# Kernel optimization log

Measured on AMD Instinct MI355X. Metric: run time of the kernel, lower is better.

Reference implementation:

```python
import jax, jax.numpy as jnp
import numpy as np

N = 50000
E = 600000
F_IN = 128      # float features (in_channels - 1)
CE = 8          # cell embedding dim
D_IN = F_IN + CE  # 136
C = 128         # out_channels
NUM_CELLS = 854
NEG_SLOPE = 0.2
LN_EPS = 1e-5


def _gat_layer(x, src, dst, W, a_src, a_dst, b):
    """PyG GATConv, heads=1, concat=False, add_self_loops already in src/dst.
    x: [N, Din]; src/dst: [Etot]; W: [Din, C]; a_src/a_dst: [C]; b: [C].
    """
    h = x @ W                               # [N, C]
    alpha_src = h @ a_src                   # [N]
    alpha_dst = h @ a_dst                   # [N]
    e = jax.nn.leaky_relu(alpha_src[src] + alpha_dst[dst], NEG_SLOPE)  # [Etot]
    # segment softmax over edges sharing a destination node
    m = jax.ops.segment_max(e, dst, num_segments=N)    # [N] (every node has a self-loop)
    ex = jnp.exp(e - m[dst])                           # [Etot]
    denom = jax.ops.segment_sum(ex, dst, num_segments=N)  # [N]
    alpha = ex / denom[dst]                            # [Etot]
    out = jax.ops.segment_sum(h[src] * alpha[:, None], dst, num_segments=N)  # [N, C]
    return out + b


def _layer_norm(x, g, b):
    mu = jnp.mean(x, axis=-1, keepdims=True)
    var = jnp.var(x, axis=-1, keepdims=True)
    return (x - mu) * jax.lax.rsqrt(var + LN_EPS) * g + b


def setup_inputs() -> dict:
    key = jax.random.key(0)
    ks = jax.random.split(key, 12)
    x_base = jax.random.normal(ks[0], (N, F_IN), dtype=jnp.float32)
    cell_ids = jax.random.randint(ks[1], (N,), 0, NUM_CELLS, dtype=jnp.int64)
    edge_index = jax.random.randint(ks[2], (2, E), 0, N, dtype=jnp.int64)
    s = 0.05
    cell_emb = jax.random.normal(ks[3], (NUM_CELLS, CE), dtype=jnp.float32)
    W1 = jax.random.normal(ks[4], (D_IN, C), dtype=jnp.float32) * s
    a_src1 = jax.random.normal(ks[5], (C,), dtype=jnp.float32) * s
    a_dst1 = jax.random.normal(ks[6], (C,), dtype=jnp.float32) * s
    b1 = jnp.zeros((C,), dtype=jnp.float32)
    ln_g = jnp.ones((C,), dtype=jnp.float32)
    ln_b = jnp.zeros((C,), dtype=jnp.float32)
    W2 = jax.random.normal(ks[7], (C, C), dtype=jnp.float32) * s
    a_src2 = jax.random.normal(ks[8], (C,), dtype=jnp.float32) * s
    a_dst2 = jax.random.normal(ks[9], (C,), dtype=jnp.float32) * s
    b2 = jnp.zeros((C,), dtype=jnp.float32)
    return {
        "x_base": x_base, "cell_ids": cell_ids, "edge_index": edge_index,
        "cell_emb": cell_emb,
        "W1": W1, "a_src1": a_src1, "a_dst1": a_dst1, "b1": b1,
        "ln_g": ln_g, "ln_b": ln_b,
        "W2": W2, "a_src2": a_src2, "a_dst2": a_dst2, "b2": b2,
    }


def reference(x_base, cell_ids, edge_index, cell_emb,
              W1, a_src1, a_dst1, b1, ln_g, ln_b,
              W2, a_src2, a_dst2, b2):
    # embed cell ids and concat (equiv. to x[:, :-1] + Embedding(x[:, -1]))
    x = jnp.concatenate([x_base, cell_emb[cell_ids]], axis=1)   # [N, 136]
    # PyG GATConv adds self-loops internally
    loops = jnp.arange(N, dtype=edge_index.dtype)
    src = jnp.concatenate([edge_index[0], loops])
    dst = jnp.concatenate([edge_index[1], loops])
    # layer 1 + LN + ELU (dropout inactive in eval mode)
    x = _gat_layer(x, src, dst, W1, a_src1, a_dst1, b1)
    x = jax.nn.elu(_layer_norm(x, ln_g, ln_b))
    # layer 2 (no norm/activation on last layer)
    x = _gat_layer(x, src, dst, W2, a_src2, a_dst2, b2)
    return x
```

## Files before the change

kernel.cpp:

```cpp
#include <hip/hip_runtime.h>
#include <hip/hip_fp16.h>
#include <cstdint>
#include <cstddef>

#define NEG_SLOPE 0.2f
#define LN_EPS 1e-5f

constexpr int BS = 256;
constexpr int EPT = 8;
constexpr int SUBCAP = 96;
constexpr int STRIDE = 96;

typedef _Float16 f16x8 __attribute__((ext_vector_type(8)));
typedef float f32x4 __attribute__((ext_vector_type(4)));

__global__ __launch_bounds__(256) void k_init(
    const int* __restrict__ esrc, const int* __restrict__ edst,
    unsigned int* __restrict__ gb, int* __restrict__ bcnt,
    const float* __restrict__ W1, const float* __restrict__ W2,
    _Float16* __restrict__ Wt1, _Float16* __restrict__ Wt2,
    int e, int nb, int nblk)
{
    int b = blockIdx.x;
    if (b < nblk) {
        __shared__ int lcnt[64];
        int tid = threadIdx.x;
        if (tid < 64) lcnt[tid] = 0;
        __syncthreads();
        int base = b * (BS * EPT) + tid;
        int sv[EPT], dl[EPT], bk[EPT], lp[EPT];
        #pragma unroll
        for (int u = 0; u < EPT; ++u) {
            int i = base + u * BS;
            bool ok = i < e;
            int ii = ok ? i : 0;
            sv[u] = esrc[ii];
            int d = edst[ii];
            dl[u] = d & 1023;
            bk[u] = ok ? (d >> 10) : -1;
        }
        #pragma unroll
        for (int u = 0; u < EPT; ++u)
            lp[u] = (bk[u] >= 0) ? atomicAdd(&lcnt[bk[u]], 1) : SUBCAP;
        __syncthreads();
        if (tid < nb) bcnt[b * nb + tid] = lcnt[tid] < SUBCAP ? lcnt[tid] : SUBCAP;
        #pragma unroll
        for (int u = 0; u < EPT; ++u)
            if (bk[u] >= 0 && lp[u] < SUBCAP)
                gb[((size_t)bk[u] * nblk + b) * SUBCAP + lp[u]] =
                    ((unsigned)dl[u] << 16) | (unsigned)sv[u];
    } else {
        int idx = (b - nblk) * BS + threadIdx.x;
        if (idx < 128 * 160) {
            int nn = idx / 160, k = idx - nn * 160;
            Wt1[idx] = (_Float16)((k < 136) ? W1[(size_t)k * 128 + nn] : 0.f);
        } else if (idx < 128 * 160 + 128 * 128) {
            int j = idx - 128 * 160;
            int nn = j >> 7, k = j & 127;
            Wt2[j] = (_Float16)W2[(size_t)k * 128 + nn];
        }
    }
}

__global__ __launch_bounds__(256) void k_csr_gemm1(
    const unsigned int* __restrict__ gb, const int* __restrict__ bcnt,
    int* __restrict__ cnt, unsigned short* __restrict__ sn,
    const float* __restrict__ x, const int* __restrict__ cid,
    const float* __restrict__ emb,
    const _Float16* __restrict__ Wt1,
    const float* __restrict__ a_src, const float* __restrict__ a_dst,
    _Float16* __restrict__ hb, float* __restrict__ as_, float* __restrict__ ad_,
    int n, int nb, int nblk)
{
    __shared__ float red[2][16][2][2];
    __shared__ int cl[1024];
    int b = blockIdx.x;

    if (b < nb) {
        int tid = threadIdx.x;
        #pragma unroll 4
        for (int i = tid; i < 1024; i += BS) cl[i] = 1;
        __syncthreads();
        for (int blk = tid; blk < nblk; blk += BS) {
            int c = bcnt[blk * nb + b];
            size_t gbase = ((size_t)b * nblk + blk) * SUBCAP;
            for (int j = 0; j < c; j += 8) {
                uint4 p0 = *(const uint4*)(gb + gbase + j);
                uint4 p1 = *(const uint4*)(gb + gbase + j + 4);
                unsigned pk[8] = {p0.x, p0.y, p0.z, p0.w, p1.x, p1.y, p1.z, p1.w};
                int slot[8];
                #pragma unroll
                for (int k = 0; k < 8; ++k)
                    slot[k] = (j + k < c) ? atomicAdd(&cl[pk[k] >> 16], 1) : STRIDE;
                #pragma unroll
                for (int k = 0; k < 8; ++k)
                    if (slot[k] < STRIDE)
                        sn[((size_t)(b * 1024 + (int)(pk[k] >> 16))) * STRIDE + slot[k]] =
                            (unsigned short)(pk[k] & 0xFFFFu);
            }
        }
        __syncthreads();
        for (int i = tid; i < 1024; i += BS) {
            int node = b * 1024 + i;
            if (node < n) {
                int c = cl[i];
                cnt[node] = c < STRIDE ? c : STRIDE;
                sn[(size_t)node * STRIDE] = (unsigned short)node;
            }
        }
        return;
    }

    int idx = b - nb;
    int tid = threadIdx.x;
    int wave = tid >> 6, lane = tid & 63;
    int rg = wave >> 1, ch = wave & 1;
    int r15 = lane & 15, q = lane >> 4;
    int rowBase = idx * 32 + rg * 16;
    int colBase = ch * 64;
    int row = rowBase + r15;
    bool ok = row < n;
    int rl = ok ? row : n - 1;

    f32x4 acc[4] = {};
    const _Float16* Wp[4];
    #pragma unroll
    for (int s = 0; s < 4; ++s)
        Wp[s] = Wt1 + (size_t)(colBase + s * 16 + r15) * 160 + q * 8;
    const float* Xp = x + (size_t)rl * 128 + q * 8;

    #pragma unroll
    for (int k0 = 0; k0 < 128; k0 += 32) {
        f16x8 wv[4];
        #pragma unroll
        for (int s = 0; s < 4; ++s) wv[s] = *(const f16x8*)(Wp[s] + k0);
        float4 xlo = *(const float4*)(Xp + k0);
        float4 xhi = *(const float4*)(Xp + k0 + 4);
        f16x8 xv;
        xv[0] = (_Float16)xlo.x; xv[1] = (_Float16)xlo.y;
        xv[2] = (_Float16)xlo.z; xv[3] = (_Float16)xlo.w;
        xv[4] = (_Float16)xhi.x; xv[5] = (_Float16)xhi.y;
        xv[6] = (_Float16)xhi.z; xv[7] = (_Float16)xhi.w;
        #pragma unroll
        for (int s = 0; s < 4; ++s)
            acc[s] = __builtin_amdgcn_mfma_f32_16x16x32_f16(wv[s], xv, acc[s], 0, 0, 0);
    }
    {
        f16x8 wv[4];
        #pragma unroll
        for (int s = 0; s < 4; ++s) wv[s] = *(const f16x8*)(Wp[s] + 128);
        f16x8 xv;
        #pragma unroll
        for (int j = 0; j < 8; ++j) xv[j] = (_Float16)0.f;
        if (q == 0) {
            const float* er = emb + (size_t)cid[rl] * 8;
            float4 e0 = *(const float4*)er;
            float4 e1 = *(const float4*)(er + 4);
            xv[0] = (_Float16)e0.x; xv[1] = (_Float16)e0.y;
            xv[2] = (_Float16)e0.z; xv[3] = (_Float16)e0.w;
            xv[4] = (_Float16)e1.x; xv[5] = (_Float16)e1.y;
            xv[6] = (_Float16)e1.z; xv[7] = (_Float16)e1.w;
        }
        #pragma unroll
        for (int s = 0; s < 4; ++s)
            acc[s] = __builtin_amdgcn_mfma_f32_16x16x32_f16(wv[s], xv, acc[s], 0, 0, 0);
    }

    float vs = 0.f, vd = 0.f;
    #pragma unroll
    for (int s = 0; s < 4; ++s) {
        float4 as4 = *(const float4*)&a_src[colBase + s * 16 + q * 4];
        float4 ad4 = *(const float4*)&a_dst[colBase + s * 16 + q * 4];
        f32x4 d = acc[s];
        vs += d[0]*as4.x + d[1]*as4.y + d[2]*as4.z + d[3]*as4.w;
        vd += d[0]*ad4.x + d[1]*ad4.y + d[2]*ad4.z + d[3]*ad4.w;
        if (ok) {
            ushort4 u;
            u.x = __half_as_ushort(__float2half_rn(d[0]));
            u.y = __half_as_ushort(__float2half_rn(d[1]));
            u.z = __half_as_ushort(__float2half_rn(d[2]));
            u.w = __half_as_ushort(__float2half_rn(d[3]));
            *(ushort4*)&hb[(size_t)row * 128 + colBase + s * 16 + q * 4] = u;
        }
    }
    vs += __shfl_xor(vs, 16); vs += __shfl_xor(vs, 32);
    vd += __shfl_xor(vd, 16); vd += __shfl_xor(vd, 32);
    if (q == 0) { red[rg][r15][ch][0] = vs; red[rg][r15][ch][1] = vd; }
    __syncthreads();
    if (ch == 0 && q == 0 && ok) {
        as_[row] = red[rg][r15][0][0] + red[rg][r15][1][0];
        ad_[row] = red[rg][r15][0][1] + red[rg][r15][1][1];
    }
}

__global__ __launch_bounds__(512, 8) void k_agg1_gemm2(
    const _Float16* __restrict__ h1, const unsigned short* __restrict__ sn,
    const int* __restrict__ cnt, const float* __restrict__ as1,
    const float* __restrict__ ad1, const float* __restrict__ b1,
    const float* __restrict__ lng, const float* __restrict__ lnb,
    const _Float16* __restrict__ Wt2,
    const float* __restrict__ a_src2, const float* __restrict__ a_dst2,
    _Float16* __restrict__ h2, float* __restrict__ as2, float* __restrict__ ad2,
    int nn)
{
    __shared__ _Float16 yt[32][144];
    __shared__ float red[2][16][4][2];
    int t = blockIdx.x;
    int tid = threadIdx.x;
    int wave = tid >> 6, lane = tid & 63;
    int l4 = lane & 15, q = lane >> 4;
    int qg = wave * 4 + q;
    int node = t * 32 + qg;
    bool valid = node < nn;
    const char* hbB = (const char*)h1;

    int len = 0; float adv = 0.f;
    if (valid) {
        len = cnt[node];
        len = len < STRIDE ? len : STRIDE;
        adv = ad1[node];
    }
    int start = node * STRIDE;
    int sub = l4 & 3;

    float acc[8] = {0.f, 0.f, 0.f, 0.f, 0.f, 0.f, 0.f, 0.f};
    float dsum = 0.f;
    for (int j = 0; j < len; j += 4) {
        int rem = len - j;
        unsigned long long s4 = *(const unsigned long long*)(sn + start + j);
        int my = (int)((s4 >> (sub * 16)) & 0xFFFFull);
        float tt = as1[my] + adv;
        tt = tt > 0.f ? tt : NEG_SLOPE * tt;
        float w = __expf(fminf(tt, 70.f));
        #pragma unroll
        for (int i = 0; i < 4; ++i) {
            if (i < rem) {
                int si = (int)((s4 >> (i * 16)) & 0xFFFFull);
                float wi = __shfl(w, (lane & 48) | i);
                f16x8 hv = *(const f16x8*)(hbB + ((size_t)si << 8) + l4 * 16);
                #pragma unroll
                for (int c = 0; c < 8; ++c)
                    acc[c] = fmaf(wi, (float)hv[c], acc[c]);
                dsum += wi;
            }
        }
    }

    if (valid) {
        float inv = 1.f / dsum;
        float4 b0 = *(const float4*)&b1[l4 * 8];
        float4 bb = *(const float4*)&b1[l4 * 8 + 4];
        float vv[8];
        vv[0] = acc[0] * inv + b0.x; vv[1] = acc[1] * inv + b0.y;
        vv[2] = acc[2] * inv + b0.z; vv[3] = acc[3] * inv + b0.w;
        vv[4] = acc[4] * inv + bb.x; vv[5] = acc[5] * inv + bb.y;
        vv[6] = acc[6] * inv + bb.z; vv[7] = acc[7] * inv + bb.w;

        float s1 = 0.f, s2 = 0.f;
        #pragma unroll
        for (int c = 0; c < 8; ++c) { s1 += vv[c]; s2 += vv[c] * vv[c]; }
        #pragma unroll
        for (int o = 1; o < 16; o <<= 1) {
            s1 += __shfl_xor(s1, o);
            s2 += __shfl_xor(s2, o);
        }
        float mean = s1 * (1.f / 128.f);
        float var  = s2 * (1.f / 128.f) - mean * mean;
        float r = rsqrtf(var + LN_EPS);
        float4 g0 = *(const float4*)&lng[l4 * 8];
        float4 g1 = *(const float4*)&lng[l4 * 8 + 4];
        float4 p0 = *(const float4*)&lnb[l4 * 8];
        float4 p1 = *(const float4*)&lnb[l4 * 8 + 4];
        float gg[8] = {g0.x, g0.y, g0.z, g0.w, g1.x, g1.y, g1.z, g1.w};
        float pp[8] = {p0.x, p0.y, p0.z, p0.w, p1.x, p1.y, p1.z, p1.w};
        f16x8 o;
        #pragma unroll
        for (int c = 0; c < 8; ++c) {
            float u = (vv[c] - mean) * r * gg[c] + pp[c];
            u = u > 0.f ? u : __expf(u) - 1.f;
            o[c] = (_Float16)u;
        }
        *(f16x8*)&yt[qg][l4 * 8] = o;
    } else {
        f16x8 z;
        #pragma unroll
        for (int c = 0; c < 8; ++c) z[c] = (_Float16)0.f;
        *(f16x8*)&yt[qg][l4 * 8] = z;
    }
    __syncthreads();

    int rg = wave >> 2, cc = wave & 3;
    int r15 = l4;
    int row = t * 32 + rg * 16 + r15;
    bool ok = row < nn;

    f32x4 acc2[2] = {};
    const _Float16* Wp[2];
    #pragma unroll
    for (int s = 0; s < 2; ++s)
        Wp[s] = Wt2 + (size_t)(cc * 32 + s * 16 + r15) * 128 + q * 8;
    const _Float16* Yp = &yt[rg * 16 + r15][q * 8];

    #pragma unroll
    for (int k0 = 0; k0 < 128; k0 += 32) {
        f16x8 wv[2];
        #pragma unroll
        for (int s = 0; s < 2; ++s) wv[s] = *(const f16x8*)(Wp[s] + k0);
        f16x8 xv = *(const f16x8*)(Yp + k0);
        #pragma unroll
        for (int s = 0; s < 2; ++s)
            acc2[s] = __builtin_amdgcn_mfma_f32_16x16x32_f16(wv[s], xv, acc2[s], 0, 0, 0);
    }

    float vs = 0.f, vd = 0.f;
    #pragma unroll
    for (int s = 0; s < 2; ++s) {
        float4 as4 = *(const float4*)&a_src2[cc * 32 + s * 16 + q * 4];
        float4 ad4 = *(const float4*)&a_dst2[cc * 32 + s * 16 + q * 4];
        f32x4 d = acc2[s];
        vs += d[0]*as4.x + d[1]*as4.y + d[2]*as4.z + d[3]*as4.w;
        vd += d[0]*ad4.x + d[1]*ad4.y + d[2]*ad4.z + d[3]*ad4.w;
        if (ok) {
            ushort4 u;
            u.x = __half_as_ushort(__float2half_rn(d[0]));
            u.y = __half_as_ushort(__float2half_rn(d[1]));
            u.z = __half_as_ushort(__float2half_rn(d[2]));
            u.w = __half_as_ushort(__float2half_rn(d[3]));
            *(ushort4*)&h2[(size_t)row * 128 + cc * 32 + s * 16 + q * 4] = u;
        }
    }
    vs += __shfl_xor(vs, 16); vs += __shfl_xor(vs, 32);
    vd += __shfl_xor(vd, 16); vd += __shfl_xor(vd, 32);
    if (q == 0) { red[rg][r15][cc][0] = vs; red[rg][r15][cc][1] = vd; }
    __syncthreads();
    if (cc == 0 && q == 0 && ok) {
        as2[row] = red[rg][r15][0][0] + red[rg][r15][1][0]
                 + red[rg][r15][2][0] + red[rg][r15][3][0];
        ad2[row] = red[rg][r15][0][1] + red[rg][r15][1][1]
                 + red[rg][r15][2][1] + red[rg][r15][3][1];
    }
}

__global__ __launch_bounds__(256) void k_agg2(
    const _Float16* __restrict__ hb, const unsigned short* __restrict__ sn,
    const int* __restrict__ cnt, const float* __restrict__ as_,
    const float* __restrict__ ad_, const float* __restrict__ bias,
    float* __restrict__ out, int n_nodes)
{
    int tid = threadIdx.x;
    int wave = tid >> 6, lane = tid & 63;
    int l4 = lane & 15, q = lane >> 4;
    int node = blockIdx.x * 16 + wave * 4 + q;
    if (node >= n_nodes) return;
    int len = cnt[node];
    len = len < STRIDE ? len : STRIDE;
    int start = node * STRIDE;
    int sub = l4 & 3;
    float adv = ad_[node];
    const char* hbB = (const char*)hb;

    float acc[8] = {0.f, 0.f, 0.f, 0.f, 0.f, 0.f, 0.f, 0.f};
    float dsum = 0.f;
    for (int j = 0; j < len; j += 4) {
        int rem = len - j;
        unsigned long long s4 = *(const unsigned long long*)(sn + start + j);
        int my = (int)((s4 >> (sub * 16)) & 0xFFFFull);
        float t = as_[my] + adv;
        t = t > 0.f ? t : NEG_SLOPE * t;
        float w = __expf(fminf(t, 70.f));
        #pragma unroll
        for (int i = 0; i < 4; ++i) {
            if (i < rem) {
                int si = (int)((s4 >> (i * 16)) & 0xFFFFull);
                float wi = __shfl(w, (lane & 48) | i);
                f16x8 hv = *(const f16x8*)(hbB + ((size_t)si << 8) + l4 * 16);
                #pragma unroll
                for (int c = 0; c < 8; ++c)
                    acc[c] = fmaf(wi, (float)hv[c], acc[c]);
                dsum += wi;
            }
        }
    }

    float inv = 1.f / dsum;
    float4 b0 = *(const float4*)&bias[l4 * 8];
    float4 b1 = *(const float4*)&bias[l4 * 8 + 4];
    float4 o0 = make_float4(acc[0]*inv + b0.x, acc[1]*inv + b0.y,
                            acc[2]*inv + b0.z, acc[3]*inv + b0.w);
    float4 o1 = make_float4(acc[4]*inv + b1.x, acc[5]*inv + b1.y,
                            acc[6]*inv + b1.z, acc[7]*inv + b1.w);
    *(float4*)(out + (size_t)node * 128 + l4 * 8)     = o0;
    *(float4*)(out + (size_t)node * 128 + l4 * 8 + 4) = o1;
}


extern "C" void kernel_launch(void* const* d_in, const int* in_sizes, int n_in,
                              void* d_out, int out_size, void* d_ws, size_t ws_size,
                              hipStream_t stream) {
    const float* x_base   = (const float*)d_in[0];
    const int*   cell_ids = (const int*)d_in[1];
    const int*   eidx     = (const int*)d_in[2];
    const float* cell_emb = (const float*)d_in[3];
    const float* W1     = (const float*)d_in[4];
    const float* a_src1 = (const float*)d_in[5];
    const float* a_dst1 = (const float*)d_in[6];
    const float* b1     = (const float*)d_in[7];
    const float* ln_g   = (const float*)d_in[8];
    const float* ln_b   = (const float*)d_in[9];
    const float* W2     = (const float*)d_in[10];
    const float* a_src2 = (const float*)d_in[11];
    const float* a_dst2 = (const float*)d_in[12];
    const float* b2     = (const float*)d_in[13];

    const int N = in_sizes[0] / 128;
    const int E = in_sizes[2] / 2;

    const int* esrc = eidx;
    const int* edst = eidx + E;

    const int NB   = (N + 1023) >> 10;
    const int NBLK = (E + BS * EPT - 1) / (BS * EPT);

    auto align = [](size_t v) { return (v + 255) & ~(size_t)255; };
    char* p = (char*)d_ws;
    int*   cnt    = (int*)p;   p += align((size_t)N * 4);
    unsigned short* sn = (unsigned short*)p; p += align((size_t)N * STRIDE * 2 + 64);
    unsigned int* gb = (unsigned int*)p; p += align((size_t)NB * NBLK * SUBCAP * 4);
    int*   bcnt   = (int*)p;   p += align((size_t)NBLK * NB * 4);
    _Float16* h1  = (_Float16*)p; p += align((size_t)N * 128 * 2);
    _Float16* h2  = (_Float16*)p; p += align((size_t)N * 128 * 2);
    _Float16* Wt1 = (_Float16*)p; p += align((size_t)128 * 160 * 2);
    _Float16* Wt2 = (_Float16*)p; p += align((size_t)128 * 128 * 2);
    float* as1    = (float*)p; p += align((size_t)N * 4);
    float* ad1    = (float*)p; p += align((size_t)N * 4);
    float* as2    = (float*)p; p += align((size_t)N * 4);
    float* ad2    = (float*)p; p += align((size_t)N * 4);
    (void)ws_size; (void)n_in; (void)out_size;

    const int nbG = (N + 31) / 32;
    const int wblocks = (128 * 160 + 128 * 128 + BS - 1) / BS;

    k_init<<<NBLK + wblocks, BS, 0, stream>>>(
        esrc, edst, gb, bcnt, W1, W2, Wt1, Wt2, E, NB, NBLK);
    k_csr_gemm1<<<NB + nbG, BS, 0, stream>>>(
        gb, bcnt, cnt, sn, x_base, cell_ids, cell_emb, Wt1,
        a_src1, a_dst1, h1, as1, ad1, N, NB, NBLK);
    k_agg1_gemm2<<<nbG, 512, 0, stream>>>(
        h1, sn, cnt, as1, ad1, b1, ln_g, ln_b, Wt2,
        a_src2, a_dst2, h2, as2, ad2, N);
    k_agg2<<<(N + 15) / 16, BS, 0, stream>>>(
        h2, sn, cnt, as2, ad2, b2, (float*)d_out, N);
}
```

Baseline: 216.9 us.

## Batch neighbor gathers in 16-edge chunks with eight loads in flight

Both aggregation kernels now compute attention weights for 16 neighbors at once (one per lane in a 16-lane group). Each batch of eight neighbor feature rows is gathered before any FMA runs, so several memory loads are in flight at the same time, replacing the previous serial 4-edge loop. Padded slots get weight zero and read row 0. Launch bounds are lowered to 4 waves per SIMD so the kernels can use more registers for the buffered loads. The cost is extra padded gather work for low-degree nodes, with at least 16 loads per node, plus lower occupancy.

```diff
diff --git a/kernel.cpp b/kernel.cpp
--- a/kernel.cpp
+++ b/kernel.cpp
@@ -13,6 +13,24 @@
 
 typedef _Float16 f16x8 __attribute__((ext_vector_type(8)));
 typedef float f32x4 __attribute__((ext_vector_type(4)));
+
+__device__ __forceinline__ void agg_half8(
+    const char* hbB, int idk, float wk, int qbase, int hoff, int l4, float acc[8])
+{
+    f16x8 hv[8];
+    #pragma unroll
+    for (int i = 0; i < 8; ++i) {
+        int si = __shfl(idk, qbase + hoff + i);
+        hv[i] = *(const f16x8*)(hbB + ((size_t)si << 8) + l4 * 16);
+    }
+    #pragma unroll
+    for (int i = 0; i < 8; ++i) {
+        float wi = __shfl(wk, qbase + hoff + i);
+        #pragma unroll
+        for (int c = 0; c < 8; ++c)
+            acc[c] = fmaf(wi, (float)hv[i][c], acc[c]);
+    }
+}
 
 __global__ __launch_bounds__(256) void k_init(
     const int* __restrict__ esrc, const int* __restrict__ edst,
@@ -193,7 +211,7 @@
     }
 }
 
-__global__ __launch_bounds__(512, 8) void k_agg1_gemm2(
+__global__ __launch_bounds__(512, 4) void k_agg1_gemm2(
     const _Float16* __restrict__ h1, const unsigned short* __restrict__ sn,
     const int* __restrict__ cnt, const float* __restrict__ as1,
     const float* __restrict__ ad1, const float* __restrict__ b1,
@@ -213,6 +231,7 @@
     int node = t * 32 + qg;
     bool valid = node < nn;
     const char* hbB = (const char*)h1;
+    int qbase = lane & 48;
 
     int len = 0; float adv = 0.f;
     if (valid) {
@@ -220,31 +239,44 @@
         len = len < STRIDE ? len : STRIDE;
         adv = ad1[node];
     }
-    int start = node * STRIDE;
-    int sub = l4 & 3;
+    int start = valid ? node * STRIDE : 0;
+
+    int id0 = sn[start + l4], id1 = sn[start + 16 + l4], id2 = sn[start + 32 + l4];
+    id0 = (l4      < len) ? id0 : 0;
+    id1 = (l4 + 16 < len) ? id1 : 0;
+    id2 = (l4 + 32 < len) ? id2 : 0;
+    float t0 = as1[id0] + adv; t0 = t0 > 0.f ? t0 : NEG_SLOPE * t0;
+    float t1 = as1[id1] + adv; t1 = t1 > 0.f ? t1 : NEG_SLOPE * t1;
+    float t2 = as1[id2] + adv; t2 = t2 > 0.f ? t2 : NEG_SLOPE * t2;
+    float w0 = (l4      < len) ? __expf(fminf(t0, 70.f)) : 0.f;
+    float w1 = (l4 + 16 < len) ? __expf(fminf(t1, 70.f)) : 0.f;
+    float w2 = (l4 + 32 < len) ? __expf(fminf(t2, 70.f)) : 0.f;
+    float wsum = w0 + w1 + w2;
 
     float acc[8] = {0.f, 0.f, 0.f, 0.f, 0.f, 0.f, 0.f, 0.f};
-    float dsum = 0.f;
-    for (int j = 0; j < len; j += 4) {
-        int rem = len - j;
-        unsigned long long s4 = *(const unsigned long long*)(sn + start + j);
-        int my = (int)((s4 >> (sub * 16)) & 0xFFFFull);
-        float tt = as1[my] + adv;
-        tt = tt > 0.f ? tt : NEG_SLOPE * tt;
-        float w = __expf(fminf(tt, 70.f));
-        #pragma unroll
-        for (int i = 0; i < 4; ++i) {
-            if (i < rem) {
-                int si = (int)((s4 >> (i * 16)) & 0xFFFFull);
-                float wi = __shfl(w, (lane & 48) | i);
-                f16x8 hv = *(const f16x8*)(hbB + ((size_t)si << 8) + l4 * 16);
-                #pragma unroll
-                for (int c = 0; c < 8; ++c)
-                    acc[c] = fmaf(wi, (float)hv[c], acc[c]);
-                dsum += wi;
-            }
-        }
-    }
+    agg_half8(hbB, id0, w0, qbase, 0, l4, acc);
+    agg_half8(hbB, id0, w0, qbase, 8, l4, acc);
+    if (len > 16) {
+        agg_half8(hbB, id1, w1, qbase, 0, l4, acc);
+        agg_half8(hbB, id1, w1, qbase, 8, l4, acc);
+    }
+    if (len > 32) {
+        agg_half8(hbB, id2, w2, qbase, 0, l4, acc);
+        agg_half8(hbB, id2, w2, qbase, 8, l4, acc);
+    }
+    for (int c = 48; c < len; c += 16) {
+        int idk = sn[start + c + l4];
+        bool a = (c + l4 < len);
+        idk = a ? idk : 0;
+        float tt = as1[idk] + adv; tt = tt > 0.f ? tt : NEG_SLOPE * tt;
+        float wk = a ? __expf(fminf(tt, 70.f)) : 0.f;
+        wsum += wk;
+        agg_half8(hbB, idk, wk, qbase, 0, l4, acc);
+        agg_half8(hbB, idk, wk, qbase, 8, l4, acc);
+    }
+    float dsum = wsum;
+    dsum += __shfl_xor(dsum, 1); dsum += __shfl_xor(dsum, 2);
+    dsum += __shfl_xor(dsum, 4); dsum += __shfl_xor(dsum, 8);
 
     if (valid) {
         float inv = 1.f / dsum;
@@ -341,7 +373,7 @@
     }
 }
 
-__global__ __launch_bounds__(256) void k_agg2(
+__global__ __launch_bounds__(256, 4) void k_agg2(
     const _Float16* __restrict__ hb, const unsigned short* __restrict__ sn,
     const int* __restrict__ cnt, const float* __restrict__ as_,
     const float* __restrict__ ad_, const float* __restrict__ bias,
@@ -355,32 +387,46 @@
     int len = cnt[node];
     len = len < STRIDE ? len : STRIDE;
     int start = node * STRIDE;
-    int sub = l4 & 3;
+    int qbase = lane & 48;
     float adv = ad_[node];
     const char* hbB = (const char*)hb;
 
+    int id0 = sn[start + l4], id1 = sn[start + 16 + l4], id2 = sn[start + 32 + l4];
+    id0 = (l4      < len) ? id0 : 0;
+    id1 = (l4 + 16 < len) ? id1 : 0;
+    id2 = (l4 + 32 < len) ? id2 : 0;
+    float t0 = as_[id0] + adv; t0 = t0 > 0.f ? t0 : NEG_SLOPE * t0;
+    float t1 = as_[id1] + adv; t1 = t1 > 0.f ? t1 : NEG_SLOPE * t1;
+    float t2 = as_[id2] + adv; t2 = t2 > 0.f ? t2 : NEG_SLOPE * t2;
+    float w0 = (l4      < len) ? __expf(fminf(t0, 70.f)) : 0.f;
+    float w1 = (l4 + 16 < len) ? __expf(fminf(t1, 70.f)) : 0.f;
+    float w2 = (l4 + 32 < len) ? __expf(fminf(t2, 70.f)) : 0.f;
+    float wsum = w0 + w1 + w2;
+
     float acc[8] = {0.f, 0.f, 0.f, 0.f, 0.f, 0.f, 0.f, 0.f};
-    float dsum = 0.f;
-    for (int j = 0; j < len; j += 4) {
-        int rem = len - j;
-        unsigned long long s4 = *(const unsigned long long*)(sn + start + j);
-        int my = (int)((s4 >> (sub * 16)) & 0xFFFFull);
-        float t = as_[my] + adv;
-        t = t > 0.f ? t : NEG_SLOPE * t;
-        float w = __expf(fminf(t, 70.f));
-        #pragma unroll
-        for (int i = 0; i < 4; ++i) {
-            if (i < rem) {
-                int si = (int)((s4 >> (i * 16)) & 0xFFFFull);
-                float wi = __shfl(w, (lane & 48) | i);
-                f16x8 hv = *(const f16x8*)(hbB + ((size_t)si << 8) + l4 * 16);
-                #pragma unroll
-                for (int c = 0; c < 8; ++c)
-                    acc[c] = fmaf(wi, (float)hv[c], acc[c]);
-                dsum += wi;
-            }
-        }
-    }
+    agg_half8(hbB, id0, w0, qbase, 0, l4, acc);
+    agg_half8(hbB, id0, w0, qbase, 8, l4, acc);
+    if (len > 16) {
+        agg_half8(hbB, id1, w1, qbase, 0, l4, acc);
+        agg_half8(hbB, id1, w1, qbase, 8, l4, acc);
+    }
+    if (len > 32) {
+        agg_half8(hbB, id2, w2, qbase, 0, l4, acc);
+        agg_half8(hbB, id2, w2, qbase, 8, l4, acc);
+    }
+    for (int c = 48; c < len; c += 16) {
+        int idk = sn[start + c + l4];
+        bool a = (c + l4 < len);
+        idk = a ? idk : 0;
+        float tt = as_[idk] + adv; tt = tt > 0.f ? tt : NEG_SLOPE * tt;
+        float wk = a ? __expf(fminf(tt, 70.f)) : 0.f;
+        wsum += wk;
+        agg_half8(hbB, idk, wk, qbase, 0, l4, acc);
+        agg_half8(hbB, idk, wk, qbase, 8, l4, acc);
+    }
+    float dsum = wsum;
+    dsum += __shfl_xor(dsum, 1); dsum += __shfl_xor(dsum, 2);
+    dsum += __shfl_xor(dsum, 4); dsum += __shfl_xor(dsum, 8);
 
     float inv = 1.f / dsum;
     float4 b0 = *(const float4*)&bias[l4 * 8];
```

New measurement: 205.9 us. -5.1%, faster.
